# Kernel optimization log

Measured on AMD Instinct MI355X. Metric: run time of the kernel, lower is better.

## Reference

```python
import jax, jax.numpy as jnp
import numpy as np

B, V, CIN, COUT, TDIM = 2, 65536, 128, 256, 512
EPS = 1e-5
G1, G2 = 32, 32  # _gn_num_groups(128)=32, _gn_num_groups(256)=32


def group_norm(x, w, b, groups):
    # x: [B, V, C]; torch GroupNorm on [B, C, V] normalizes per (batch, group)
    # over the group's channels AND all V positions (biased variance).
    Bx, Vx, C = x.shape
    xr = x.reshape(Bx, Vx, groups, C // groups)
    mean = xr.mean(axis=(1, 3), keepdims=True)
    var = xr.var(axis=(1, 3), keepdims=True)
    xn = ((xr - mean) * jax.lax.rsqrt(var + EPS)).reshape(Bx, Vx, C)
    return xn * w + b


def neigh_conv(x, neigh, W, b):
    # x: [B, V, C]; neigh: [V, 9]; W: [out, 9*C]; b: [out]
    C = x.shape[-1]
    gathered = x[:, neigh]                      # [B, V, 9, C]
    Wr = W.reshape(-1, 9, C)                    # [out, 9, C]
    return jnp.einsum('bvnc,onc->bvo', gathered, Wr) + b


def setup_inputs() -> dict:
    key = jax.random.key(0)
    ks = jax.random.split(key, 12)
    s = 0.02
    return {
        'x': jax.random.normal(ks[0], (B, V, CIN), jnp.float32),
        't_emb': jax.random.normal(ks[1], (B, TDIM), jnp.float32),
        'neigh_orders': jax.random.randint(ks[2], (V, 9), 0, V, jnp.int64)
            if jax.config.jax_enable_x64 else jax.random.randint(ks[2], (V, 9), 0, V, jnp.int32),
        'gn1_w': jnp.ones((CIN,), jnp.float32),
        'gn1_b': jnp.zeros((CIN,), jnp.float32),
        'w1': jax.random.normal(ks[3], (COUT, 9 * CIN), jnp.float32) * s,
        'b1': jnp.zeros((COUT,), jnp.float32),
        'wt': jax.random.normal(ks[4], (COUT, TDIM), jnp.float32) * s,
        'bt': jnp.zeros((COUT,), jnp.float32),
        'gn2_w': jnp.ones((COUT,), jnp.float32),
        'gn2_b': jnp.zeros((COUT,), jnp.float32),
        'w2': jax.random.normal(ks[5], (COUT, 9 * COUT), jnp.float32) * s,
        'b2': jnp.zeros((COUT,), jnp.float32),
        'ws': jax.random.normal(ks[6], (COUT, CIN), jnp.float32) * s,
        'bs': jnp.zeros((COUT,), jnp.float32),
    }


def reference(x, t_emb, neigh_orders, gn1_w, gn1_b, w1, b1, wt, bt,
              gn2_w, gn2_b, w2, b2, ws, bs):
    h = group_norm(x, gn1_w, gn1_b, G1)
    h = jax.nn.silu(h)
    h = neigh_conv(h, neigh_orders, w1, b1)                 # [B, V, COUT]
    t = jax.nn.silu(t_emb) @ wt.T + bt                      # [B, COUT]
    h = h + t[:, None, :]
    h = group_norm(h, gn2_w, gn2_b, G2)
    h = jax.nn.silu(h)
    h = neigh_conv(h, neigh_orders, w2, b2)                 # [B, V, COUT]
    shortcut = x @ ws.T + bs                                # learned 1x1 (in_ch != out_ch)
    return h + shortcut
```

## Files before the change

### kernel.cpp

```cpp
#include <hip/hip_runtime.h>
#include <hip/hip_bf16.h>

#define DEV __device__ __forceinline__

typedef __attribute__((ext_vector_type(8))) short bf16x8;
typedef __attribute__((ext_vector_type(4))) float f32x4;

constexpr int Bb = 2, V = 65536, CIN = 128, COUT = 256, TDIM = 512;
constexpr float EPS = 1e-5f;
constexpr int K1 = 1152, K2 = 2304, K2e = 2432;
constexpr int NCH1 = 128;
constexpr int NCH2 = 256;
constexpr int W1N = (K1/8)*COUT*8;
constexpr int W2N = (K2e/8)*COUT*8;

DEV float silu_f(float x){ return x / (1.f + __expf(-x)); }
DEV unsigned short f2b(float x){
  union { float f; unsigned u; } v; v.f = x;
  unsigned r = v.u + 0x7fffu + ((v.u >> 16) & 1u);
  return (unsigned short)(r >> 16);
}
DEV float b2f(unsigned short h){ union { unsigned u; float f; } v; v.u = ((unsigned)h) << 16; return v.f; }

__global__ void k_gn1_partial(const float* __restrict__ x, float* __restrict__ part){
  int b = blockIdx.y, ch = blockIdx.x;
  int t = threadIdx.x;
  int c = t & 127;
  int r0 = t >> 7;
  float s = 0.f, ss = 0.f;
  const float* xp = x + ((size_t)b*V + (size_t)ch*512)*CIN + c;
  for (int r = r0; r < 512; r += 2){
    float v = xp[(size_t)r*CIN];
    s += v; ss += v*v;
  }
  __shared__ float s_s[256], s_q[256];
  s_s[t] = s; s_q[t] = ss; __syncthreads();
  if (t < 128){ s_s[t] += s_s[t+128]; s_q[t] += s_q[t+128]; }
  __syncthreads();
  if (t < 32){
    float a = 0, q = 0;
    for (int i = 0; i < 4; ++i){ a += s_s[t*4+i]; q += s_q[t*4+i]; }
    int idx = ((b*32 + t)*NCH1 + ch)*2;
    part[idx] = a; part[idx+1] = q;
  }
}

__global__ void k_gn1_final(const float* __restrict__ part, const float* __restrict__ w,
                            const float* __restrict__ bias, float* __restrict__ sc,
                            float* __restrict__ bi){
  int t = threadIdx.x;
  if (t >= Bb*32) return;
  float s = 0, q = 0;
  for (int ch = 0; ch < NCH1; ++ch){ s += part[(t*NCH1+ch)*2]; q += part[(t*NCH1+ch)*2+1]; }
  float n = (float)V * 4.f;
  float mean = s / n;
  float var = q / n - mean*mean;
  float inv = rsqrtf(var + EPS);
  int b = t >> 5, g = t & 31;
  for (int j = 0; j < 4; ++j){
    int c = g*4 + j;
    float scl = w[c] * inv;
    sc[b*CIN + c] = scl;
    bi[b*CIN + c] = bias[c] - mean*scl;
  }
}

__global__ void k_act1(const float* __restrict__ x, const float* __restrict__ sc,
                       const float* __restrict__ bi, unsigned short* __restrict__ act1,
                       unsigned short* __restrict__ xb){
  size_t i = ((size_t)blockIdx.x*256 + threadIdx.x)*4;
  int c = (int)(i & (CIN-1));
  int b = (int)(i >> 23);
  float4 v = *(const float4*)(x + i);
  const float* scp = sc + b*CIN + c;
  const float* bip = bi + b*CIN + c;
  ushort4 a, xo;
  a.x = f2b(silu_f(v.x*scp[0] + bip[0]));
  a.y = f2b(silu_f(v.y*scp[1] + bip[1]));
  a.z = f2b(silu_f(v.z*scp[2] + bip[2]));
  a.w = f2b(silu_f(v.w*scp[3] + bip[3]));
  xo.x = f2b(v.x); xo.y = f2b(v.y); xo.z = f2b(v.z); xo.w = f2b(v.w);
  *(ushort4*)(act1 + i) = a;
  *(ushort4*)(xb + i)   = xo;
}

__global__ void k_prepW(const float* __restrict__ w1, const float* __restrict__ w2,
                        const float* __restrict__ wsm, unsigned short* __restrict__ W1b,
                        unsigned short* __restrict__ W2b){
  int i = blockIdx.x*256 + threadIdx.x;
  if (i < W1N){
    int j = i & 7, o = (i >> 3) & 255, k8 = i >> 11;
    W1b[i] = f2b(w1[o*K1 + k8*8 + j]);
  }
  int i2 = i - W1N;
  if (i2 >= 0 && i2 < W2N){
    int j = i2 & 7, o = (i2 >> 3) & 255, k8 = i2 >> 11;
    int k = k8*8 + j;
    float v = (k < K2) ? w2[o*K2 + k] : wsm[o*CIN + (k - K2)];
    W2b[i2] = f2b(v);
  }
}

__global__ void k_tcomb(const float* __restrict__ temb, const float* __restrict__ wt,
                        const float* __restrict__ bt, const float* __restrict__ b1,
                        float* __restrict__ tc){
  int b = blockIdx.y;
  int o = blockIdx.x*4 + (threadIdx.x >> 6);
  int l = threadIdx.x & 63;
  const float* tb = temb + (size_t)b*TDIM;
  const float* wr = wt + (size_t)o*TDIM;
  float acc = 0.f;
  #pragma unroll
  for (int k = l; k < TDIM; k += 64)
    acc += silu_f(tb[k]) * wr[k];
  #pragma unroll
  for (int off = 32; off > 0; off >>= 1) acc += __shfl_down(acc, off, 64);
  if (l == 0) tc[b*COUT + o] = acc + bt[o] + b1[o];
}

template<int CINR, int NCHUNK, int CPN, bool CONV2>
__launch_bounds__(256, 4)
__global__ void k_conv(const unsigned short* __restrict__ act,
                       const unsigned short* __restrict__ xb,
                       const unsigned short* __restrict__ Wb,
                       const int* __restrict__ neigh,
                       const float* __restrict__ tc,
                       const float* __restrict__ b2,
                       const float* __restrict__ bs,
                       unsigned short* __restrict__ outb,
                       float* __restrict__ outf){
  __shared__ __align__(16) unsigned short A_lds[128*64];
  __shared__ int nb[128*9];
  const int tid = threadIdx.x;
  const int w = tid >> 6, lane = tid & 63;
  const int d = blockIdx.x;
  const int bx = ((d >> 4) << 3) + (d & 7);
  const int n0 = ((d >> 3) & 1) << 7;
  const int vflat = bx << 7;
  const int b = vflat >> 16;
  const int vb = vflat & (V-1);
  for (int i = tid; i < 128*9; i += 256) nb[i] = neigh[(size_t)vb*9 + i];

  f32x4 acc[4][4] = {};
  const int wm = w >> 1, wn = w & 1;
  const int quad = lane >> 4, l15 = lane & 15;
  const int sr = lane >> 3, ssg = lane & 7;

  const unsigned short* actb = act + (size_t)b*V*CINR;
  const unsigned short* xbb  = CONV2 ? (xb + (size_t)b*V*CIN) : (const unsigned short*)nullptr;
  const unsigned short* wq = Wb + (size_t)quad*COUT*8 + (size_t)(n0 + (wn<<6) + l15)*8;

  __syncthreads();

  #pragma unroll 1
  for (int chunk = 0; chunk < NCHUNK; ++chunk){
    {
      const bool scseg = CONV2 && (chunk >= NCHUNK-2);
      int nidx = 0, c0, rl;
      const unsigned short* src;
      if (scseg){ c0 = (chunk - (NCHUNK-2))*64; src = xbb; rl = CIN; }
      else      { nidx = chunk / CPN; c0 = (chunk % CPN)*64; src = actb; rl = CINR; }
      #pragma unroll
      for (int i = 0; i < 4; ++i){
        int row  = (w<<5) + (i<<3) + sr;
        int rowg = scseg ? (vb + row) : nb[row*9 + nidx];
        int g = ssg ^ (row & 7);
        const unsigned short* gp = src + (size_t)rowg*rl + c0 + g*8;
        unsigned short* lp = A_lds + (((w<<5) + (i<<3))<<6);
        __builtin_amdgcn_global_load_lds(gp, lp, 16, 0, 0);
      }
    }
    bf16x8 bv[8];
    {
      const unsigned short* wp = wq + (size_t)chunk*8*COUT*8;
      #pragma unroll
      for (int nt = 0; nt < 4; ++nt){
        bv[nt*2+0] = *(const bf16x8*)(wp + (nt<<7));
        bv[nt*2+1] = *(const bf16x8*)(wp + 4*COUT*8 + (nt<<7));
      }
    }
    __syncthreads();

    __builtin_amdgcn_s_setprio(1);
    #pragma unroll
    for (int ks = 0; ks < 2; ++ks){
      bf16x8 av[4];
      #pragma unroll
      for (int mt = 0; mt < 4; ++mt){
        int m = (wm<<6) + (mt<<4) + l15;
        int seg = ((ks<<2) + quad) ^ (l15 & 7);
        av[mt] = *(const bf16x8*)&A_lds[(m<<6) + (seg<<3)];
      }
      #pragma unroll
      for (int mt = 0; mt < 4; ++mt)
        #pragma unroll
        for (int nt = 0; nt < 4; ++nt)
          acc[mt][nt] = __builtin_amdgcn_mfma_f32_16x16x32_bf16(av[mt], bv[nt*2+ks], acc[mt][nt], 0, 0, 0);
    }
    __builtin_amdgcn_s_setprio(0);
    __syncthreads();
  }

  #pragma unroll
  for (int mt = 0; mt < 4; ++mt){
    #pragma unroll
    for (int nt = 0; nt < 4; ++nt){
      int col = n0 + (wn<<6) + (nt<<4) + l15;
      float bval = CONV2 ? (b2[col] + bs[col]) : tc[b*COUT + col];
      #pragma unroll
      for (int rg = 0; rg < 4; ++rg){
        int row = (wm<<6) + (mt<<4) + (quad<<2) + rg;
        size_t off = ((size_t)(vflat + row))*COUT + col;
        float v = acc[mt][nt][rg] + bval;
        if (CONV2) outf[off] = v;
        else       outb[off] = f2b(v);
      }
    }
  }
}

__global__ void k_gn2_partial(const unsigned short* __restrict__ h1, float* __restrict__ part){
  int b = blockIdx.y, ch = blockIdx.x;
  int t = threadIdx.x;
  float s = 0.f, ss = 0.f;
  const unsigned short* p = h1 + ((size_t)b*V + (size_t)ch*256)*COUT + t;
  for (int r = 0; r < 256; ++r){
    float v = b2f(p[(size_t)r*COUT]);
    s += v; ss += v*v;
  }
  __shared__ float s_s[256], s_q[256];
  s_s[t] = s; s_q[t] = ss; __syncthreads();
  if (t < 32){
    float a = 0, q = 0;
    for (int i = 0; i < 8; ++i){ a += s_s[t*8+i]; q += s_q[t*8+i]; }
    int idx = ((b*32 + t)*NCH2 + ch)*2;
    part[idx] = a; part[idx+1] = q;
  }
}

__global__ void k_gn2_final(const float* __restrict__ part, const float* __restrict__ w,
                            const float* __restrict__ bias, float* __restrict__ sc,
                            float* __restrict__ bi){
  int t = threadIdx.x;
  if (t >= Bb*32) return;
  float s = 0, q = 0;
  for (int ch = 0; ch < NCH2; ++ch){ s += part[(t*NCH2+ch)*2]; q += part[(t*NCH2+ch)*2+1]; }
  float n = (float)V * 8.f;
  float mean = s / n, var = q / n - mean*mean, inv = rsqrtf(var + EPS);
  int b = t >> 5, g = t & 31;
  for (int j = 0; j < 8; ++j){
    int c = g*8 + j;
    float scl = w[c] * inv;
    sc[b*COUT + c] = scl;
    bi[b*COUT + c] = bias[c] - mean*scl;
  }
}

__global__ void k_act2(unsigned short* __restrict__ h1, const float* __restrict__ sc,
                       const float* __restrict__ bi){
  size_t i = ((size_t)blockIdx.x*256 + threadIdx.x)*4;
  int c = (int)(i & (COUT-1));
  int b = (int)(i >> 24);
  ushort4 h = *(ushort4*)(h1 + i);
  const float* scp = sc + b*COUT + c;
  const float* bip = bi + b*COUT + c;
  ushort4 o;
  o.x = f2b(silu_f(b2f(h.x)*scp[0] + bip[0]));
  o.y = f2b(silu_f(b2f(h.y)*scp[1] + bip[1]));
  o.z = f2b(silu_f(b2f(h.z)*scp[2] + bip[2]));
  o.w = f2b(silu_f(b2f(h.w)*scp[3] + bip[3]));
  *(ushort4*)(h1 + i) = o;
}

extern "C" void kernel_launch(void* const* d_in, const int* in_sizes, int n_in,
                              void* d_out, int out_size, void* d_ws, size_t ws_size,
                              hipStream_t stream){
  const float* x    = (const float*)d_in[0];
  const float* temb = (const float*)d_in[1];
  const int*   neigh= (const int*)d_in[2];
  const float* gn1w = (const float*)d_in[3];
  const float* gn1b = (const float*)d_in[4];
  const float* w1   = (const float*)d_in[5];
  const float* b1   = (const float*)d_in[6];
  const float* wt   = (const float*)d_in[7];
  const float* bt   = (const float*)d_in[8];
  const float* gn2w = (const float*)d_in[9];
  const float* gn2b = (const float*)d_in[10];
  const float* w2   = (const float*)d_in[11];
  const float* b2   = (const float*)d_in[12];
  const float* wsm  = (const float*)d_in[13];
  const float* bs   = (const float*)d_in[14];
  float* out = (float*)d_out;

  char* wsp = (char*)d_ws;
  unsigned short* act1 = (unsigned short*)(wsp);
  unsigned short* xb   = (unsigned short*)(wsp + 33554432);
  unsigned short* h1   = (unsigned short*)(wsp + 67108864);
  unsigned short* W1b  = (unsigned short*)(wsp + 134217728);
  unsigned short* W2b  = (unsigned short*)(wsp + 134217728 + 589824);
  char* p = wsp + 134217728 + 589824 + 1245184;
  float* tc    = (float*)p;  p += 2048;
  float* part1 = (float*)p;  p += (size_t)Bb*32*NCH1*2*4;
  float* part2 = (float*)p;  p += (size_t)Bb*32*NCH2*2*4;
  float* sc1   = (float*)p;  p += 1024;
  float* bi1   = (float*)p;  p += 1024;
  float* sc2   = (float*)p;  p += 2048;
  float* bi2   = (float*)p;  p += 2048;

  k_gn1_partial<<<dim3(NCH1, Bb), 256, 0, stream>>>(x, part1);
  k_gn1_final  <<<1, 64, 0, stream>>>(part1, gn1w, gn1b, sc1, bi1);
  k_act1       <<<16384, 256, 0, stream>>>(x, sc1, bi1, act1, xb);
  k_prepW      <<<(W1N + W2N)/256, 256, 0, stream>>>(w1, w2, wsm, W1b, W2b);
  k_tcomb      <<<dim3(COUT/4, Bb), 256, 0, stream>>>(temb, wt, bt, b1, tc);
  k_conv<128, 18, 2, false><<<2048, 256, 0, stream>>>(act1, nullptr, W1b, neigh, tc, nullptr, nullptr, h1, nullptr);
  k_gn2_partial<<<dim3(NCH2, Bb), 256, 0, stream>>>(h1, part2);
  k_gn2_final  <<<1, 64, 0, stream>>>(part2, gn2w, gn2b, sc2, bi2);
  k_act2       <<<32768, 256, 0, stream>>>(h1, sc2, bi2);
  k_conv<256, 38, 4, true><<<2048, 256, 0, stream>>>(h1, xb, W2b, neigh, nullptr, b2, bs, nullptr, out);
}
```

Measured before the change: 625.2 us.

## Double-buffer the gathered A tile in LDS to overlap loads with MFMA

Splits the A shared-memory tile into two buffers and restructures the chunk loop into a software pipeline. The gather of chunk t+1 into the other buffer is issued before the MFMAs on chunk t run. Explicit vmcnt waits and raw s_barrier calls replace the two __syncthreads per chunk, so each chunk only waits for its own tile. The aim is to hide the latency of the neighbor gather behind compute. In exchange, LDS use roughly doubles, which could limit blocks per CU, and correctness now depends on the hand-counted vmcnt values.

```diff
diff --git a/kernel.cpp b/kernel.cpp
--- a/kernel.cpp
+++ b/kernel.cpp
@@ -129,7 +129,7 @@
                        const float* __restrict__ bs,
                        unsigned short* __restrict__ outb,
                        float* __restrict__ outf){
-  __shared__ __align__(16) unsigned short A_lds[128*64];
+  __shared__ __align__(16) unsigned short A_lds[2][128*64];
   __shared__ int nb[128*9];
   const int tid = threadIdx.x;
   const int w = tid >> 6, lane = tid & 63;
@@ -150,37 +150,33 @@
   const unsigned short* xbb  = CONV2 ? (xb + (size_t)b*V*CIN) : (const unsigned short*)nullptr;
   const unsigned short* wq = Wb + (size_t)quad*COUT*8 + (size_t)(n0 + (wn<<6) + l15)*8;
 
-  __syncthreads();
-
-  #pragma unroll 1
-  for (int chunk = 0; chunk < NCHUNK; ++chunk){
-    {
-      const bool scseg = CONV2 && (chunk >= NCHUNK-2);
-      int nidx = 0, c0, rl;
-      const unsigned short* src;
-      if (scseg){ c0 = (chunk - (NCHUNK-2))*64; src = xbb; rl = CIN; }
-      else      { nidx = chunk / CPN; c0 = (chunk % CPN)*64; src = actb; rl = CINR; }
-      #pragma unroll
-      for (int i = 0; i < 4; ++i){
-        int row  = (w<<5) + (i<<3) + sr;
-        int rowg = scseg ? (vb + row) : nb[row*9 + nidx];
-        int g = ssg ^ (row & 7);
-        const unsigned short* gp = src + (size_t)rowg*rl + c0 + g*8;
-        unsigned short* lp = A_lds + (((w<<5) + (i<<3))<<6);
-        __builtin_amdgcn_global_load_lds(gp, lp, 16, 0, 0);
-      }
+  auto STAGE_A = [&](int chunk, int buf){
+    const bool scseg = CONV2 && (chunk >= NCHUNK-2);
+    int nidx = 0, c0, rl;
+    const unsigned short* src;
+    if (scseg){ c0 = (chunk - (NCHUNK-2))*64; src = xbb; rl = CIN; }
+    else      { nidx = chunk / CPN; c0 = (chunk % CPN)*64; src = actb; rl = CINR; }
+    #pragma unroll
+    for (int i = 0; i < 4; ++i){
+      int row  = (w<<5) + (i<<3) + sr;
+      int rowg = scseg ? (vb + row) : nb[row*9 + nidx];
+      int g = ssg ^ (row & 7);
+      const unsigned short* gp = src + (size_t)rowg*rl + c0 + g*8;
+      unsigned short* lp = &A_lds[buf][((w<<5) + (i<<3))<<6];
+      __builtin_amdgcn_global_load_lds(gp, lp, 16, 0, 0);
     }
-    bf16x8 bv[8];
-    {
-      const unsigned short* wp = wq + (size_t)chunk*8*COUT*8;
-      #pragma unroll
-      for (int nt = 0; nt < 4; ++nt){
-        bv[nt*2+0] = *(const bf16x8*)(wp + (nt<<7));
-        bv[nt*2+1] = *(const bf16x8*)(wp + 4*COUT*8 + (nt<<7));
-      }
+  };
+
+  auto LOADB = [&](int chunk, bf16x8 (&bv)[8]){
+    const unsigned short* wp = wq + (size_t)chunk*8*COUT*8;
+    #pragma unroll
+    for (int nt = 0; nt < 4; ++nt){
+      bv[nt*2+0] = *(const bf16x8*)(wp + (nt<<7));
+      bv[nt*2+1] = *(const bf16x8*)(wp + 4*COUT*8 + (nt<<7));
     }
-    __syncthreads();
-
+  };
+
+  auto COMPUTE = [&](int cur, bf16x8 (&bv)[8]){
     __builtin_amdgcn_s_setprio(1);
     #pragma unroll
     for (int ks = 0; ks < 2; ++ks){
@@ -189,7 +185,7 @@
       for (int mt = 0; mt < 4; ++mt){
         int m = (wm<<6) + (mt<<4) + l15;
         int seg = ((ks<<2) + quad) ^ (l15 & 7);
-        av[mt] = *(const bf16x8*)&A_lds[(m<<6) + (seg<<3)];
+        av[mt] = *(const bf16x8*)&A_lds[cur][(m<<6) + (seg<<3)];
       }
       #pragma unroll
       for (int mt = 0; mt < 4; ++mt)
@@ -198,7 +194,32 @@
           acc[mt][nt] = __builtin_amdgcn_mfma_f32_16x16x32_bf16(av[mt], bv[nt*2+ks], acc[mt][nt], 0, 0, 0);
     }
     __builtin_amdgcn_s_setprio(0);
-    __syncthreads();
+  };
+
+  __syncthreads();
+  STAGE_A(0, 0);
+
+  #pragma unroll 1
+  for (int t = 0; t < NCHUNK-1; ++t){
+    const int cur = t & 1;
+    bf16x8 bv[8];
+    LOADB(t, bv);
+    STAGE_A(t+1, cur^1);
+    asm volatile("s_waitcnt vmcnt(12)" ::: "memory");
+    __builtin_amdgcn_s_barrier();
+    asm volatile("" ::: "memory");
+    COMPUTE(cur, bv);
+    asm volatile("" ::: "memory");
+    __builtin_amdgcn_s_barrier();
+    asm volatile("" ::: "memory");
+  }
+  {
+    bf16x8 bv[8];
+    LOADB(NCHUNK-1, bv);
+    asm volatile("s_waitcnt vmcnt(8)" ::: "memory");
+    __builtin_amdgcn_s_barrier();
+    asm volatile("" ::: "memory");
+    COMPUTE((NCHUNK-1) & 1, bv);
   }
 
   #pragma unroll
```

New measurement: 601.2 us. 1.04x faster.
